# Performance work log

Hardware: AMD Instinct MI355X
Metric: run time of the kernel (lower is better)

## Reference

```python
import jax, jax.numpy as jnp
import numpy as np

N, D, E = 16384, 2048, 64          # tokens, d_model, n_experts
G = 8                               # n_expert_group
TOP_K = 8                           # experts selected per token
TOP_K_GROUP = 4                     # groups selected per token


def setup_inputs() -> dict:
    key = jax.random.key(0)
    k1, k2 = jax.random.split(key)
    x = jax.random.normal(k1, (N, D), dtype=jnp.float32)
    W = jax.random.normal(k2, (E, D), dtype=jnp.float32) * 0.02  # Linear weight
    b = jnp.zeros((E,), dtype=jnp.float32)                        # Linear bias
    bias = jnp.zeros((1, E), dtype=jnp.float32)                   # aux-loss-free routing bias
    return {"x": x, "W": W, "b": b, "bias": bias}


def reference(x, W, b, bias):
    n = x.shape[0]
    # linear + sigmoid
    score2weights = jax.nn.sigmoid(x @ W.T + b)       # [N, E]
    score = score2weights + bias                      # routing score with bias
    # group view
    score_g = score.reshape(n, G, -1)                 # [N, G, E/G]
    w_g = score2weights.reshape(n, G, -1)
    # group score = sum of top min(2, top_k) expert scores within each group
    top2, _ = jax.lax.top_k(score_g, min(2, TOP_K))   # [N, G, 2]
    group_score = top2.sum(axis=-1)                   # [N, G]
    # select top groups, build group mask (scatter)
    _, gidx = jax.lax.top_k(group_score, TOP_K_GROUP) # [N, TOP_K_GROUP]
    mask = jnp.zeros((n, G), score.dtype).at[jnp.arange(n)[:, None], gidx].set(1.0)
    # mask out non-selected groups, flatten back to expert dim
    score_m = (score_g * mask[..., None]).reshape(n, -1)   # [N, E]
    w_m = (w_g * mask[..., None]).reshape(n, -1)
    # final per-token expert selection + weight gather
    _, idx = jax.lax.top_k(score_m, TOP_K)            # [N, TOP_K] int32
    weights = jnp.take_along_axis(w_m, idx, axis=1)   # [N, TOP_K]
    return weights, idx
```

## Files before the change

### kernel.cpp

```cpp
#include <hip/hip_runtime.h>
#include <math.h>

#define DIM   2048
#define NEXP  64
#define NGRP  8
#define GSIZE 8
#define TOPK  8
#define TOPKG 4

#define TPB1  1024
#define NKS   8
#define KSL   (DIM / NKS)
#define SMSTR 1092

#define TAU_E 6e-5f
#define TAU_G 1.2e-4f
#define NEG_INF (-3.4e38f)
#define WLOFF 16
#define WT_OFF (1 << 18)

typedef __attribute__((ext_vector_type(8)))  _Float16 f16x8;
typedef __attribute__((ext_vector_type(16))) float    f32x16;

#define SB() __builtin_amdgcn_sched_barrier(0)
#define WAITVM(n) asm volatile("s_waitcnt vmcnt(" #n ")" ::: "memory")

static __device__ __forceinline__ void gload_lds16(const void* g, void* l) {
    __builtin_amdgcn_global_load_lds(
        (const __attribute__((address_space(1))) unsigned*)g,
        (__attribute__((address_space(3))) unsigned*)l,
        16, 0, 0);
}

__global__ __launch_bounds__(256) void prep_kernel(
    const float* __restrict__ W, unsigned short* __restrict__ Wf,
    int* __restrict__ wl)
{
    const int g = blockIdx.x * 256 + threadIdx.x;
    const int e = g >> 11, k = g & 2047;
    const float w = W[g];
    const _Float16 hi = (_Float16)w;
    const _Float16 lo = (_Float16)(w - (float)hi);
    const int n2 = e >> 5, lcol = e & 31;
    const int kc = k >> 4, khalf = (k >> 3) & 1, j = k & 7;
    const int lane = (khalf << 5) | lcol;
    Wf[((((0 * 2 + n2) * 128 + kc) << 6) + lane) * 8 + j] =
        __builtin_bit_cast(unsigned short, hi);
    Wf[((((1 * 2 + n2) * 128 + kc) << 6) + lane) * 8 + j] =
        __builtin_bit_cast(unsigned short, lo);
    if (g < WLOFF) wl[g] = 0;
}

__global__ __launch_bounds__(TPB1, 4) void gate_kernel(
    const float* __restrict__ x,
    const unsigned short* __restrict__ Wf,
    const float* __restrict__ b,
    const float* __restrict__ bias,
    float* __restrict__ out_w,
    float* __restrict__ out_i,
    int* __restrict__ wl)
{
    __shared__ __align__(16) char sLDS[65536];
    float* sM = (float*)sLDS;
    float (*sS)[65] = (float (*)[65])(sLDS + 34944);

    const int tid  = threadIdx.x;
    const int w    = tid >> 6;
    const int lane = tid & 63;
    const int m    = w >> 3;
    const int ks   = w & 7;
    const int tok0 = blockIdx.x * 64;
    const int l31  = lane & 31, lh = lane >> 5;
    const int roff = (blockIdx.x >> 3) & 15;

    const float* xr = x + (size_t)(tok0 + 32 * m + l31) * DIM + ks * KSL + lh * 8;
    const char* Wfb = (const char*)Wf;

    f32x16 acc0, acc1;
#pragma unroll
    for (int z = 0; z < 16; ++z) { acc0[z] = 0.f; acc1[z] = 0.f; }

#define STAGE_B(tt, cc) do {                                                  \
        char* dst_ = sLDS + (((tt) & 1) ? 32768 : 0) + ks * 4096;             \
        const int kc_ = ks * 16 + (cc);                                       \
        gload_lds16(Wfb + (size_t)((0 * 128 + kc_) * 64 + lane) * 16, dst_);  \
        gload_lds16(Wfb + (size_t)((1 * 128 + kc_) * 64 + lane) * 16, dst_ + 1024); \
        gload_lds16(Wfb + (size_t)((2 * 128 + kc_) * 64 + lane) * 16, dst_ + 2048); \
        gload_lds16(Wfb + (size_t)((3 * 128 + kc_) * 64 + lane) * 16, dst_ + 3072); \
    } while (0)

    float4 pA[3], pB[3];
    {
        const int cc0 = roff;
        pA[0] = *(const float4*)(xr + cc0 * 16);
        pB[0] = *(const float4*)(xr + cc0 * 16 + 4);
        SB();
        if (m == 0) STAGE_B(0, cc0);
        SB();
        const int cc1 = (1 + roff) & 15;
        pA[1] = *(const float4*)(xr + cc1 * 16);
        pB[1] = *(const float4*)(xr + cc1 * 16 + 4);
        SB();
    }

#pragma unroll
    for (int t = 0; t < 16; ++t) {
        if (t + 1 < 16) {
            const int cc1 = (t + 1 + roff) & 15;
            if (m == 0) STAGE_B(t + 1, cc1);
        }
        SB();
        if (t + 2 < 16) {
            const int cc2 = (t + 2 + roff) & 15;
            pA[(t + 2) % 3] = *(const float4*)(xr + cc2 * 16);
            pB[(t + 2) % 3] = *(const float4*)(xr + cc2 * 16 + 4);
        }
        if (t <= 13)      WAITVM(8);
        else if (t == 14) WAITVM(6);
        else              WAITVM(0);
        SB();
        __builtin_amdgcn_s_barrier();
        SB();

        const char* src = sLDS + ((t & 1) ? 32768 : 0) + ks * 4096;
        const f16x8 bh0 = *(const f16x8*)(src + 0 * 1024 + lane * 16);
        const f16x8 bh1 = *(const f16x8*)(src + 1 * 1024 + lane * 16);
        const f16x8 bl0 = *(const f16x8*)(src + 2 * 1024 + lane * 16);
        const f16x8 bl1 = *(const f16x8*)(src + 3 * 1024 + lane * 16);
        const float4 qa = pA[t % 3], qb = pB[t % 3];
        const float xv[8] = {qa.x, qa.y, qa.z, qa.w, qb.x, qb.y, qb.z, qb.w};
        f16x8 ah, al;
#pragma unroll
        for (int j = 0; j < 8; j += 2) {
            const auto h2 = __builtin_amdgcn_cvt_pkrtz(xv[j], xv[j + 1]);
            const auto l2 = __builtin_amdgcn_cvt_pkrtz(xv[j]     - (float)h2.x,
                                                       xv[j + 1] - (float)h2.y);
            ah[j] = h2.x; ah[j + 1] = h2.y;
            al[j] = l2.x; al[j + 1] = l2.y;
        }
        acc0 = __builtin_amdgcn_mfma_f32_32x32x16_f16(ah, bh0, acc0, 0, 0, 0);
        acc0 = __builtin_amdgcn_mfma_f32_32x32x16_f16(ah, bl0, acc0, 0, 0, 0);
        acc0 = __builtin_amdgcn_mfma_f32_32x32x16_f16(al, bh0, acc0, 0, 0, 0);
        acc1 = __builtin_amdgcn_mfma_f32_32x32x16_f16(ah, bh1, acc1, 0, 0, 0);
        acc1 = __builtin_amdgcn_mfma_f32_32x32x16_f16(ah, bl1, acc1, 0, 0, 0);
        acc1 = __builtin_amdgcn_mfma_f32_32x32x16_f16(al, bh1, acc1, 0, 0, 0);
        SB();
        __builtin_amdgcn_s_barrier();
        SB();
    }
#undef STAGE_B

#pragma unroll
    for (int r = 0; r < 4; ++r) {
#pragma unroll
        for (int jj = 0; jj < 4; ++jj) {
            const int t16 = 8 * m + jj + 4 * lh;
            sM[ks * SMSTR + t16 * 68 + l31]      = acc0[4 * r + jj];
            sM[ks * SMSTR + t16 * 68 + l31 + 32] = acc1[4 * r + jj];
        }
        __syncthreads();
        {
            const int t16 = tid >> 6;
            const int e   = tid & 63;
            float sum = 0.f;
#pragma unroll
            for (int s = 0; s < NKS; ++s)
                sum += sM[s * SMSTR + t16 * 68 + e];
            const float logit = sum + b[e];
            const float wv = 1.0f / (1.0f + expf(-logit));
            const int t_blk = 32 * (t16 >> 3) + 8 * r + (t16 & 7);
            sS[t_blk][e] = wv + bias[e];
        }
        __syncthreads();
    }

    if (tid < 64) {
        const int t = tid;

        float gs[NGRP];
#pragma unroll
        for (int g = 0; g < NGRP; ++g) {
            float m1 = NEG_INF, m2 = NEG_INF;
#pragma unroll
            for (int j = 0; j < GSIZE; ++j) {
                const float v = sS[t][g * GSIZE + j];
                if (v > m1) { m2 = m1; m1 = v; }
                else if (v > m2) { m2 = v; }
            }
            gs[g] = m1 + m2;
        }

        unsigned gmask = 0u;
        float g4val = NEG_INF;
        for (int rr = 0; rr < TOPKG; ++rr) {
            float best = NEG_INF; int bi = 0;
#pragma unroll
            for (int g = 0; g < NGRP; ++g) {
                const float v = ((gmask >> g) & 1u) ? NEG_INF : gs[g];
                if (v > best) { best = v; bi = g; }
            }
            gmask |= 1u << bi;
            g4val = best;
        }
        float m5 = NEG_INF;
#pragma unroll
        for (int g = 0; g < NGRP; ++g)
            if (!((gmask >> g) & 1u) && gs[g] > m5) m5 = gs[g];
        const float margin_g = g4val - m5;

        unsigned long long chosen = 0ull;
        const size_t obase = (size_t)(tok0 + t) * TOPK;
        float vals[TOPK + 1];
        for (int rr = 0; rr < TOPK + 1; ++rr) {
            float best = NEG_INF; int bi = 0;
            for (int e = 0; e < NEXP; ++e) {
                float v = ((gmask >> (e >> 3)) & 1u) ? sS[t][e] : 0.0f;
                if ((chosen >> e) & 1ull) v = NEG_INF;
                if (v > best) { best = v; bi = e; }
            }
            vals[rr] = best;
            if (rr < TOPK) {
                chosen |= 1ull << (unsigned)bi;
                out_w[obase + rr] = ((gmask >> (bi >> 3)) & 1u)
                                  ? (sS[t][bi] - bias[bi]) : 0.0f;
                out_i[obase + rr] = (float)bi;
            }
        }
        float margin_e = 1e30f;
#pragma unroll
        for (int rr = 0; rr < TOPK; ++rr) {
            const float d = vals[rr] - vals[rr + 1];
            if (d < margin_e) margin_e = d;
        }

        if (margin_g < TAU_G || margin_e < TAU_E) {
            const int slot = atomicAdd(wl, 1);
            wl[WLOFF + slot] = tok0 + t;
        }
    }
}

__global__ __launch_bounds__(256) void gate_fix_kernel(
    const float* __restrict__ x,
    const float* __restrict__ W,
    const float* __restrict__ b,
    const float* __restrict__ bias,
    float* __restrict__ out_w,
    float* __restrict__ out_i,
    const int* __restrict__ wl)
{
    const int count = wl[0];

    __shared__ __align__(16) float sX[DIM];
    __shared__ double sPart[NEXP][4];
    __shared__ float  sS2[NEXP], sW2[NEXP];

    const int tid = threadIdx.x;
    const int e   = tid >> 2;
    const int s   = tid & 3;

    for (int widx = blockIdx.x; widx < count; widx += (int)gridDim.x) {
        const int tok = wl[WLOFF + widx];

        const float4* xr = (const float4*)(x + (size_t)tok * DIM);
        ((float4*)sX)[tid]       = xr[tid];
        ((float4*)sX)[tid + 256] = xr[tid + 256];
        __syncthreads();

        const float4* Wr = (const float4*)(W + (size_t)e * DIM);
        double a0 = 0., a1 = 0., a2 = 0., a3 = 0.;
#pragma unroll 8
        for (int mm = 0; mm < DIM / 16; ++mm) {
            const int c = mm * 4 + s;
            const float4 wv = Wr[c];
            const float4 xv = ((const float4*)sX)[c];
            a0 = fma((double)xv.x, (double)wv.x, a0);
            a1 = fma((double)xv.y, (double)wv.y, a1);
            a2 = fma((double)xv.z, (double)wv.z, a2);
            a3 = fma((double)xv.w, (double)wv.w, a3);
        }
        sPart[e][s] = (a0 + a1) + (a2 + a3);
        __syncthreads();

        if (tid < NEXP) {
            const double logit = ((sPart[tid][0] + sPart[tid][1])
                                + (sPart[tid][2] + sPart[tid][3])) + (double)b[tid];
            const float wv = (float)(1.0 / (1.0 + exp(-logit)));
            sW2[tid] = wv;
            sS2[tid] = wv + bias[tid];
        }
        __syncthreads();

        if (tid == 0) {
            float gs[NGRP];
#pragma unroll
            for (int g = 0; g < NGRP; ++g) {
                float m1 = NEG_INF, m2 = NEG_INF;
#pragma unroll
                for (int j = 0; j < GSIZE; ++j) {
                    const float v = sS2[g * GSIZE + j];
                    if (v > m1) { m2 = m1; m1 = v; }
                    else if (v > m2) { m2 = v; }
                }
                gs[g] = m1 + m2;
            }
            unsigned gmask = 0u;
            for (int rr = 0; rr < TOPKG; ++rr) {
                float best = NEG_INF; int bi = 0;
#pragma unroll
                for (int g = 0; g < NGRP; ++g) {
                    const float v = ((gmask >> g) & 1u) ? NEG_INF : gs[g];
                    if (v > best) { best = v; bi = g; }
                }
                gmask |= 1u << bi;
            }
            unsigned long long chosen = 0ull;
            const size_t obase = (size_t)tok * TOPK;
            for (int rr = 0; rr < TOPK; ++rr) {
                float best = NEG_INF; int bi = 0;
                for (int e2 = 0; e2 < NEXP; ++e2) {
                    float v = ((gmask >> (e2 >> 3)) & 1u) ? sS2[e2] : 0.0f;
                    if ((chosen >> e2) & 1ull) v = NEG_INF;
                    if (v > best) { best = v; bi = e2; }
                }
                chosen |= 1ull << (unsigned)bi;
                out_w[obase + rr] = ((gmask >> (bi >> 3)) & 1u) ? sW2[bi] : 0.0f;
                out_i[obase + rr] = (float)bi;
            }
        }
        __syncthreads();
    }
}

extern "C" void kernel_launch(void* const* d_in, const int* in_sizes, int n_in,
                              void* d_out, int out_size, void* d_ws, size_t ws_size,
                              hipStream_t stream) {
    const float* x    = (const float*)d_in[0];
    const float* W    = (const float*)d_in[1];
    const float* b    = (const float*)d_in[2];
    const float* bias = (const float*)d_in[3];

    const int n = in_sizes[0] / DIM;
    float* out_w = (float*)d_out;
    float* out_i = out_w + (size_t)n * TOPK;
    int*   wl    = (int*)d_ws;
    unsigned short* Wf = (unsigned short*)((char*)d_ws + WT_OFF);

    prep_kernel<<<dim3((NEXP * DIM) / 256), dim3(256), 0, stream>>>(W, Wf, wl);
    gate_kernel<<<dim3(n / 64), dim3(TPB1), 0, stream>>>(
        x, Wf, b, bias, out_w, out_i, wl);
    gate_fix_kernel<<<dim3(1024), dim3(256), 0, stream>>>(
        x, W, b, bias, out_w, out_i, wl);
}
```

Measured before the change: 274.3 us.

## Stage x tiles through LDS with swizzle, load W fragments directly

Swaps the staging roles. x tiles for the block are now copied into double-buffered LDS with direct global-to-LDS loads using an XOR swizzle, in contiguous 128-float row chunks per iteration. The f16 hi/lo W fragments are read straight from global memory into registers, where before they went through LDS. The intent is coalesced, contiguous x reads with fewer strided per-thread loads, at the cost of W coming from L2 without LDS sharing and a different pipelining depth.

```diff
diff --git a/kernel.cpp b/kernel.cpp
--- a/kernel.cpp
+++ b/kernel.cpp
@@ -10,7 +10,6 @@
 
 #define TPB1  1024
 #define NKS   8
-#define KSL   (DIM / NKS)
 #define SMSTR 1092
 
 #define TAU_E 6e-5f
@@ -71,84 +70,74 @@
     const int ks   = w & 7;
     const int tok0 = blockIdx.x * 64;
     const int l31  = lane & 31, lh = lane >> 5;
-    const int roff = (blockIdx.x >> 3) & 15;
-
-    const float* xr = x + (size_t)(tok0 + 32 * m + l31) * DIM + ks * KSL + lh * 8;
+
     const char* Wfb = (const char*)Wf;
+    const char* xb  = (const char*)x;
 
     f32x16 acc0, acc1;
 #pragma unroll
     for (int z = 0; z < 16; ++z) { acc0[z] = 0.f; acc1[z] = 0.f; }
 
-#define STAGE_B(tt, cc) do {                                                  \
-        char* dst_ = sLDS + (((tt) & 1) ? 32768 : 0) + ks * 4096;             \
-        const int kc_ = ks * 16 + (cc);                                       \
-        gload_lds16(Wfb + (size_t)((0 * 128 + kc_) * 64 + lane) * 16, dst_);  \
-        gload_lds16(Wfb + (size_t)((1 * 128 + kc_) * 64 + lane) * 16, dst_ + 1024); \
-        gload_lds16(Wfb + (size_t)((2 * 128 + kc_) * 64 + lane) * 16, dst_ + 2048); \
-        gload_lds16(Wfb + (size_t)((3 * 128 + kc_) * 64 + lane) * 16, dst_ + 3072); \
-    } while (0)
-
-    float4 pA[3], pB[3];
-    {
-        const int cc0 = roff;
-        pA[0] = *(const float4*)(xr + cc0 * 16);
-        pB[0] = *(const float4*)(xr + cc0 * 16 + 4);
-        SB();
-        if (m == 0) STAGE_B(0, cc0);
-        SB();
-        const int cc1 = (1 + roff) & 15;
-        pA[1] = *(const float4*)(xr + cc1 * 16);
-        pB[1] = *(const float4*)(xr + cc1 * 16 + 4);
+#define STAGE_X(Mn) do {                                                      \
+        char* dst_ = sLDS + (((Mn) & 1) ? 32768 : 0);                         \
+        _Pragma("unroll")                                                     \
+        for (int o_ = 0; o_ < 2; ++o_) {                                      \
+            const int ra_  = 4 * w + 2 * o_;                                  \
+            const int row_ = ra_ + lh;                                        \
+            const int sw_  = (row_ & 7) << 4;                                 \
+            const size_t src_ = (size_t)(tok0 + row_) * (DIM * 4)             \
+                              + (size_t)(Mn) * 512 + ((l31 * 16) ^ sw_);      \
+            gload_lds16(xb + src_, dst_ + ra_ * 512);                         \
+        } } while (0)
+
+    STAGE_X(0);
+    WAITVM(0);
+    __builtin_amdgcn_s_barrier();
+    SB();
+
+    for (int M = 0; M < 16; ++M) {
+        if (M < 15) STAGE_X(M + 1);
+        SB();
+        const int kc = 8 * M + ks;
+        const f16x8 bh0 = *(const f16x8*)(Wfb + (size_t)((0 * 128 + kc) * 64 + lane) * 16);
+        const f16x8 bh1 = *(const f16x8*)(Wfb + (size_t)((1 * 128 + kc) * 64 + lane) * 16);
+        const f16x8 bl0 = *(const f16x8*)(Wfb + (size_t)((2 * 128 + kc) * 64 + lane) * 16);
+        const f16x8 bl1 = *(const f16x8*)(Wfb + (size_t)((3 * 128 + kc) * 64 + lane) * 16);
+        SB();
+        if (M < 15) { WAITVM(6); } else { WAITVM(4); }
+        SB();
+        __builtin_amdgcn_s_barrier();
+        SB();
+
+        {
+            const char* pb = sLDS + ((M & 1) ? 32768 : 0)
+                           + (32 * m + l31) * 512;
+            const int sw   = ((32 * m + l31) & 7) << 4;
+            const int colb = 64 * ks + 32 * lh;
+            const float4 fa = *(const float4*)(pb + ((colb)      ^ sw));
+            const float4 fb = *(const float4*)(pb + ((colb + 16) ^ sw));
+            const float xv[8] = {fa.x, fa.y, fa.z, fa.w, fb.x, fb.y, fb.z, fb.w};
+            f16x8 ah, al;
+#pragma unroll
+            for (int j = 0; j < 8; j += 2) {
+                const auto h2 = __builtin_amdgcn_cvt_pkrtz(xv[j], xv[j + 1]);
+                const auto l2 = __builtin_amdgcn_cvt_pkrtz(xv[j]     - (float)h2.x,
+                                                           xv[j + 1] - (float)h2.y);
+                ah[j] = h2.x; ah[j + 1] = h2.y;
+                al[j] = l2.x; al[j + 1] = l2.y;
+            }
+            acc0 = __builtin_amdgcn_mfma_f32_32x32x16_f16(ah, bh0, acc0, 0, 0, 0);
+            acc0 = __builtin_amdgcn_mfma_f32_32x32x16_f16(ah, bl0, acc0, 0, 0, 0);
+            acc0 = __builtin_amdgcn_mfma_f32_32x32x16_f16(al, bh0, acc0, 0, 0, 0);
+            acc1 = __builtin_amdgcn_mfma_f32_32x32x16_f16(ah, bh1, acc1, 0, 0, 0);
+            acc1 = __builtin_amdgcn_mfma_f32_32x32x16_f16(ah, bl1, acc1, 0, 0, 0);
+            acc1 = __builtin_amdgcn_mfma_f32_32x32x16_f16(al, bh1, acc1, 0, 0, 0);
+        }
+        SB();
+        __builtin_amdgcn_s_barrier();
         SB();
     }
-
-#pragma unroll
-    for (int t = 0; t < 16; ++t) {
-        if (t + 1 < 16) {
-            const int cc1 = (t + 1 + roff) & 15;
-            if (m == 0) STAGE_B(t + 1, cc1);
-        }
-        SB();
-        if (t + 2 < 16) {
-            const int cc2 = (t + 2 + roff) & 15;
-            pA[(t + 2) % 3] = *(const float4*)(xr + cc2 * 16);
-            pB[(t + 2) % 3] = *(const float4*)(xr + cc2 * 16 + 4);
-        }
-        if (t <= 13)      WAITVM(8);
-        else if (t == 14) WAITVM(6);
-        else              WAITVM(0);
-        SB();
-        __builtin_amdgcn_s_barrier();
-        SB();
-
-        const char* src = sLDS + ((t & 1) ? 32768 : 0) + ks * 4096;
-        const f16x8 bh0 = *(const f16x8*)(src + 0 * 1024 + lane * 16);
-        const f16x8 bh1 = *(const f16x8*)(src + 1 * 1024 + lane * 16);
-        const f16x8 bl0 = *(const f16x8*)(src + 2 * 1024 + lane * 16);
-        const f16x8 bl1 = *(const f16x8*)(src + 3 * 1024 + lane * 16);
-        const float4 qa = pA[t % 3], qb = pB[t % 3];
-        const float xv[8] = {qa.x, qa.y, qa.z, qa.w, qb.x, qb.y, qb.z, qb.w};
-        f16x8 ah, al;
-#pragma unroll
-        for (int j = 0; j < 8; j += 2) {
-            const auto h2 = __builtin_amdgcn_cvt_pkrtz(xv[j], xv[j + 1]);
-            const auto l2 = __builtin_amdgcn_cvt_pkrtz(xv[j]     - (float)h2.x,
-                                                       xv[j + 1] - (float)h2.y);
-            ah[j] = h2.x; ah[j + 1] = h2.y;
-            al[j] = l2.x; al[j + 1] = l2.y;
-        }
-        acc0 = __builtin_amdgcn_mfma_f32_32x32x16_f16(ah, bh0, acc0, 0, 0, 0);
-        acc0 = __builtin_amdgcn_mfma_f32_32x32x16_f16(ah, bl0, acc0, 0, 0, 0);
-        acc0 = __builtin_amdgcn_mfma_f32_32x32x16_f16(al, bh0, acc0, 0, 0, 0);
-        acc1 = __builtin_amdgcn_mfma_f32_32x32x16_f16(ah, bh1, acc1, 0, 0, 0);
-        acc1 = __builtin_amdgcn_mfma_f32_32x32x16_f16(ah, bl1, acc1, 0, 0, 0);
-        acc1 = __builtin_amdgcn_mfma_f32_32x32x16_f16(al, bh1, acc1, 0, 0, 0);
-        SB();
-        __builtin_amdgcn_s_barrier();
-        SB();
-    }
-#undef STAGE_B
+#undef STAGE_X
 
 #pragma unroll
     for (int r = 0; r < 4; ++r) {
```

Measured after the change: 271.0 us. No clear change (-1.2%).
